# Kernel tuning notes

Measured on AMD Instinct MI355X. Metric: run time of the kernel, lower is better.

The kernel has to match this reference:

```python
import jax, jax.numpy as jnp
import numpy as np

B, SA, SB, H, D = 1, 2048, 512, 24, 128
DIM = H * D
EPS = 1e-6


def rms_norm(x, w):
    # fp32 variance as in the torch module (inputs already fp32 here)
    var = jnp.mean(jnp.square(x.astype(jnp.float32)), axis=-1, keepdims=True)
    y = (x * jax.lax.rsqrt(var + EPS)).astype(x.dtype)
    return y * w


def apply_rope(x, freqs):
    # x: [B,H,S,D]; freqs: [1,1,S,D/2,2,2]
    x_ = x.astype(jnp.float32).reshape(*x.shape[:-1], -1, 1, 2)  # [B,H,S,D/2,1,2]
    out = freqs[..., 0] * x_[..., 0] + freqs[..., 1] * x_[..., 1]  # [B,H,S,D/2,2]
    return out.reshape(x.shape).astype(x.dtype)


def qkv_split(x, W, b):
    # x: [B,S,DIM] -> q,k,v each [B,H,S,D]; chunk(3,dim=1) on 3H axis == major-3 split
    qkv = (x @ W + b).reshape(x.shape[0], x.shape[1], 3, H, D)
    qkv = jnp.transpose(qkv, (2, 0, 3, 1, 4))  # [3,B,H,S,D]
    return qkv[0], qkv[1], qkv[2]


def setup_inputs():
    key = jax.random.key(0)
    ks = jax.random.split(key, 8)
    s = 0.02
    return {
        "hidden_states_a": jax.random.normal(ks[0], (B, SA, DIM), jnp.float32),
        "hidden_states_b": jax.random.normal(ks[1], (B, SB, DIM), jnp.float32),
        "image_rotary_emb": jax.random.normal(ks[2], (1, 1, SA + SB, D // 2, 2, 2), jnp.float32),
        "Wqkv_a": jax.random.normal(ks[3], (DIM, 3 * DIM), jnp.float32) * s,
        "bqkv_a": jnp.zeros((3 * DIM,), jnp.float32),
        "Wqkv_b": jax.random.normal(ks[4], (DIM, 3 * DIM), jnp.float32) * s,
        "bqkv_b": jnp.zeros((3 * DIM,), jnp.float32),
        "wq_a": jnp.ones((D,), jnp.float32),
        "wk_a": jnp.ones((D,), jnp.float32),
        "wq_b": jnp.ones((D,), jnp.float32),
        "wk_b": jnp.ones((D,), jnp.float32),
        "Wout_a": jax.random.normal(ks[5], (DIM, DIM), jnp.float32) * s,
        "bout_a": jnp.zeros((DIM,), jnp.float32),
        "Wout_b": jax.random.normal(ks[6], (DIM, DIM), jnp.float32) * s,
        "bout_b": jnp.zeros((DIM,), jnp.float32),
    }


def reference(hidden_states_a, hidden_states_b, image_rotary_emb,
              Wqkv_a, bqkv_a, Wqkv_b, bqkv_b,
              wq_a, wk_a, wq_b, wk_b,
              Wout_a, bout_a, Wout_b, bout_b):
    q_a, k_a, v_a = qkv_split(hidden_states_a, Wqkv_a, bqkv_a)
    q_a, k_a = rms_norm(q_a, wq_a), rms_norm(k_a, wk_a)
    q_b, k_b, v_b = qkv_split(hidden_states_b, Wqkv_b, bqkv_b)
    q_b, k_b = rms_norm(q_b, wq_b), rms_norm(k_b, wk_b)

    q = jnp.concatenate([q_b, q_a], axis=2)
    k = jnp.concatenate([k_b, k_a], axis=2)
    v = jnp.concatenate([v_b, v_a], axis=2)
    q, k = apply_rope(q, image_rotary_emb), apply_rope(k, image_rotary_emb)

    scale = 1.0 / jnp.sqrt(jnp.asarray(D, q.dtype))
    scores = jnp.einsum("bhqd,bhkd->bhqk", q, k) * scale
    attn = jax.nn.softmax(scores, axis=-1)
    out = jnp.einsum("bhqk,bhkd->bhqd", attn, v)
    out = jnp.transpose(out, (0, 2, 1, 3)).reshape(B, SA + SB, DIM)

    out_b, out_a = out[:, :SB], out[:, SB:]
    hidden_states_a = out_a @ Wout_a + bout_a
    hidden_states_b = out_b @ Wout_b + bout_b
    return hidden_states_a, hidden_states_b
```

## Files before the change

kernel.cpp:

```cpp
#include <hip/hip_runtime.h>
#include <hip/hip_bf16.h>


typedef __attribute__((ext_vector_type(8))) short s16x8;
typedef __attribute__((ext_vector_type(8))) unsigned short u16x8;
typedef __attribute__((ext_vector_type(4))) unsigned short u16x4;
typedef __attribute__((ext_vector_type(4))) float f32x4;
typedef __attribute__((ext_vector_type(16))) float f32x16;

#define DEV static __device__ __forceinline__

#define S_TOT 2560
#define DIMC 3072
#define NQKV 9216

DEV unsigned short f2bf(float f) {
  union { float f; unsigned u; } v; v.f = f;
  return (unsigned short)((v.u + 0x7fffu + ((v.u >> 16) & 1u)) >> 16);
}
DEV float bf2f(unsigned short h) {
  union { unsigned u; float f; } v; v.u = ((unsigned)h) << 16;
  return v.f;
}
DEV void gload16(const void* g, void* l) {
  __builtin_amdgcn_global_load_lds((__attribute__((address_space(1))) void*)g,
                                   (__attribute__((address_space(3))) void*)l,
                                   16, 0, 0);
}
template <int N>
DEV void wait_vm() { asm volatile("s_waitcnt vmcnt(%0)" :: "n"(N) : "memory"); }
DEV float exp2_fast(float x) {
#if __has_builtin(__builtin_amdgcn_exp2f)
  return __builtin_amdgcn_exp2f(x);
#else
  return __expf(x * 0.69314718056f);
#endif
}

DEV void tile_map(int t, int mgrid, int* m, int* n) {
  int sg = t >> 4, loc = t & 15;
  int mgs = mgrid >> 2;
  int mg = sg % mgs, ng = sg / mgs;
  *m = mg * 4 + (loc & 3);
  *n = ng * 4 + (loc >> 2);
}


__global__ __launch_bounds__(256) void prep_all(
    const float* __restrict__ Wqa, const float* __restrict__ Wqb,
    const float* __restrict__ Woa, const float* __restrict__ Wob,
    const float* __restrict__ Xa, const float* __restrict__ Xb,
    unsigned short* __restrict__ Tqa, unsigned short* __restrict__ Tqb,
    unsigned short* __restrict__ Toa, unsigned short* __restrict__ Tob,
    unsigned short* __restrict__ Oa, unsigned short* __restrict__ Ob,
    int n8a, int n8b) {
  int id = blockIdx.x;
  if (id >= 18432) {
    int i = (id - 18432) * 256 + threadIdx.x;
    const float* in; unsigned short* out;
    if (i < n8a) { in = Xa; out = Oa; }
    else { i -= n8a; if (i >= n8b) return; in = Xb; out = Ob; }
    const float4* p = (const float4*)(in + (size_t)i * 8);
    float4 a = p[0], b = p[1];
    u16x8 u;
    u[0] = f2bf(a.x); u[1] = f2bf(a.y); u[2] = f2bf(a.z); u[3] = f2bf(a.w);
    u[4] = f2bf(b.x); u[5] = f2bf(b.y); u[6] = f2bf(b.z); u[7] = f2bf(b.w);
    *(u16x8*)(out + (size_t)i * 8) = u;
    return;
  }
  __shared__ float tile[64][65];
  const float* W; unsigned short* WT; int N, ncols;
  if (id < 6912)        { W = Wqa; WT = Tqa; N = NQKV; ncols = 144; }
  else if (id < 13824)  { W = Wqb; WT = Tqb; N = NQKV; ncols = 144; id -= 6912; }
  else if (id < 16128)  { W = Woa; WT = Toa; N = DIMC; ncols = 48;  id -= 13824; }
  else                  { W = Wob; WT = Tob; N = DIMC; ncols = 48;  id -= 16128; }
  const int t = threadIdx.x;
  const int n0 = (id % ncols) * 64, k0 = (id / ncols) * 64;
#pragma unroll
  for (int rep = 0; rep < 4; ++rep) {
    int idx = rep * 256 + t;
    int r = idx >> 4, c4 = (idx & 15) * 4;
    float4 v = *(const float4*)&W[(size_t)(k0 + r) * N + n0 + c4];
    tile[r][c4] = v.x; tile[r][c4 + 1] = v.y; tile[r][c4 + 2] = v.z; tile[r][c4 + 3] = v.w;
  }
  __syncthreads();
#pragma unroll
  for (int rep = 0; rep < 2; ++rep) {
    int idx = rep * 256 + t;
    int j = idx >> 3, i0 = (idx & 7) * 8;
    u16x8 u;
#pragma unroll
    for (int i = 0; i < 8; i++) u[i] = f2bf(tile[i0 + i][j]);
    *(u16x8*)&WT[(size_t)(n0 + j) * DIMC + k0 + i0] = u;
  }
}


struct StageSmem {
  unsigned short A[128 * 64];
  unsigned short B[128 * 64];
};

DEV void stage_tile(const char* A, const char* B, StageSmem* s, int kt, int tid) {
  const int row_s = tid >> 3;
  const int kbp = (tid & 7) * 16;
#pragma unroll
  for (int st = 0; st < 4; ++st) {
    int row = st * 32 + row_s;
    int kb = kbp ^ ((row & 7) << 4);
    gload16(A + (size_t)row * (DIMC * 2) + kt * 128 + kb, (char*)s->A + st * 4096 + tid * 16);
    gload16(B + (size_t)row * (DIMC * 2) + kt * 128 + kb, (char*)s->B + st * 4096 + tid * 16);
  }
}

DEV void compute_tile(const StageSmem* s, int wr, int wc, int lh, int ll,
                      f32x4 (&acc)[4][4]) {
#pragma unroll
  for (int ks = 0; ks < 2; ++ks) {
    s16x8 a[4], b[4];
#pragma unroll
    for (int f = 0; f < 4; ++f) {
      int ar = wr * 64 + f * 16 + ll;
      a[f] = *(const s16x8*)((const char*)s->A + ar * 128 +
                             ((ks * 64 + lh * 16) ^ ((ar & 7) << 4)));
      int br = wc * 64 + f * 16 + ll;
      b[f] = *(const s16x8*)((const char*)s->B + br * 128 +
                             ((ks * 64 + lh * 16) ^ ((br & 7) << 4)));
    }
#pragma unroll
    for (int i = 0; i < 4; i++)
#pragma unroll
      for (int j = 0; j < 4; j++)
        acc[i][j] = __builtin_amdgcn_mfma_f32_16x16x32_bf16(a[i], b[j], acc[i][j], 0, 0, 0);
  }
}

DEV void gemm_core_db(const unsigned short* __restrict__ Ap,
                      const unsigned short* __restrict__ Bp,
                      StageSmem (&sm)[2], int tid, f32x4 (&acc)[4][4]) {
  const int wave = tid >> 6, lane = tid & 63;
  const int wr = wave >> 1, wc = wave & 1;
  const int lh = lane >> 4, ll = lane & 15;

  stage_tile((const char*)Ap, (const char*)Bp, &sm[0], 0, tid);
  __syncthreads();
  for (int kt = 0; kt < 48; ++kt) {
    if (kt + 1 < 48)
      stage_tile((const char*)Ap, (const char*)Bp, &sm[(kt + 1) & 1], kt + 1, tid);
    compute_tile(&sm[kt & 1], wr, wc, lh, ll, acc);
    __syncthreads();
  }
}


union QkvSmem {
  StageSmem st[2];
  unsigned short ctile[128 * 136];
};

__global__ __launch_bounds__(256, 2) void qkv_gemm(
    const unsigned short* __restrict__ X0, const unsigned short* __restrict__ X1,
    const unsigned short* __restrict__ W0, const unsigned short* __restrict__ W1,
    const float* __restrict__ b0, const float* __restrict__ b1,
    const float* __restrict__ wqa, const float* __restrict__ wka,
    const float* __restrict__ wqb, const float* __restrict__ wkb,
    const float* __restrict__ freqs,
    unsigned short* __restrict__ Qb, unsigned short* __restrict__ Kb,
    unsigned short* __restrict__ Vt, int nt0) {
  __shared__ QkvSmem sm;
  const int tid = threadIdx.x;

  const int chunk = gridDim.x >> 3;
  const int nid = ((int)blockIdx.x & 7) * chunk + ((int)blockIdx.x >> 3);
  const int strm = (nid >= nt0) ? 1 : 0;
  const int t = strm ? nid - nt0 : nid;
  int mt, nt;
  tile_map(t, strm ? 4 : 16, &mt, &nt);
  const int m0 = mt * 128, n0 = nt * 128;
  const unsigned short* Xp = (strm ? X1 : X0) + (size_t)m0 * DIMC;
  const unsigned short* Wp = (strm ? W1 : W0) + (size_t)n0 * DIMC;
  const float* biasp = (strm ? b1 : b0);
  const int s_off = strm ? 0 : 512;

  f32x4 acc[4][4] = {};
  gemm_core_db(Xp, Wp, sm.st, tid, acc);

  {
    const int wave = tid >> 6, lane = tid & 63;
    const int wr = wave >> 1, wc = wave & 1, lh = lane >> 4, ll = lane & 15;
#pragma unroll
    for (int fn = 0; fn < 4; ++fn) {
      int c = wc * 64 + fn * 16 + ll;
      float bv = biasp[n0 + c];
#pragma unroll
      for (int fm = 0; fm < 4; ++fm)
#pragma unroll
        for (int j = 0; j < 4; j++) {
          int r = wr * 64 + fm * 16 + lh * 4 + j;
          sm.ctile[r * 136 + c] = f2bf(acc[fm][fn][j] + bv);
        }
    }
  }
  __syncthreads();

  const int qkv_idx = nt / 24;
  const int head = nt % 24;

  if (qkv_idx == 2) {
    const int sg0 = s_off + m0;
#pragma unroll
    for (int half = 0; half < 2; ++half) {
      int d = half * 64 + (tid >> 2);
      int t0 = (tid & 3) * 32;
      size_t obase = (size_t)(head * 128 + d) * S_TOT + sg0 + t0;
#pragma unroll
      for (int v = 0; v < 4; ++v) {
        u16x8 u;
#pragma unroll
        for (int i = 0; i < 8; i++) u[i] = sm.ctile[(t0 + v * 8 + i) * 136 + d];
        *(u16x8*)&Vt[obase + v * 8] = u;
      }
    }
  } else {
    const float* wn = (qkv_idx == 0) ? (strm ? wqb : wqa) : (strm ? wkb : wka);
    unsigned short* Ob = (qkv_idx == 0) ? Qb : Kb;
    const int row = tid >> 1, half = tid & 1;
    const int sg = s_off + m0 + row;
    float x[64];
    float ss = 0.f;
#pragma unroll
    for (int i = 0; i < 64; i++) {
      float v = bf2f(sm.ctile[row * 136 + half * 64 + i]);
      x[i] = v; ss += v * v;
    }
    ss += __shfl_xor(ss, 1);
    const float rn = rsqrtf(ss * (1.f / 128.f) + 1e-6f);
    const float* fr = freqs + (size_t)sg * 256 + half * 128;
    unsigned short o[64];
#pragma unroll
    for (int p = 0; p < 32; ++p) {
      float w0 = wn[half * 64 + 2 * p], w1 = wn[half * 64 + 2 * p + 1];
      float y0 = x[2 * p] * rn * w0, y1 = x[2 * p + 1] * rn * w1;
      float f00 = fr[p * 4], f01 = fr[p * 4 + 1], f10 = fr[p * 4 + 2], f11 = fr[p * 4 + 3];
      o[2 * p] = f2bf(f00 * y0 + f01 * y1);
      o[2 * p + 1] = f2bf(f10 * y0 + f11 * y1);
    }
    size_t ob = ((size_t)head * S_TOT + sg) * 128 + half * 64;
#pragma unroll
    for (int v = 0; v < 8; ++v) {
      u16x8 u;
#pragma unroll
      for (int i = 0; i < 8; i++) u[i] = o[v * 8 + i];
      *(u16x8*)&Ob[ob + v * 8] = u;
    }
  }
}


__global__ __launch_bounds__(256, 2) void out_gemm(
    const unsigned short* __restrict__ A0, const unsigned short* __restrict__ A1,
    const unsigned short* __restrict__ W0, const unsigned short* __restrict__ W1,
    const float* __restrict__ b0, const float* __restrict__ b1,
    float* __restrict__ C0, float* __restrict__ C1, int nt0) {
  __shared__ StageSmem sm[2];
  const int tid = threadIdx.x;
  const int chunk = gridDim.x >> 3;
  const int nid = ((int)blockIdx.x & 7) * chunk + ((int)blockIdx.x >> 3);
  const int strm = (nid >= nt0) ? 1 : 0;
  const int t = strm ? nid - nt0 : nid;
  int mt, nt;
  tile_map(t, strm ? 4 : 16, &mt, &nt);
  const int m0 = mt * 128, n0 = nt * 128;
  const unsigned short* Ap = (strm ? A1 : A0) + (size_t)m0 * DIMC;
  const unsigned short* Wp = (strm ? W1 : W0) + (size_t)n0 * DIMC;
  const float* bias = strm ? b1 : b0;
  float* C = strm ? C1 : C0;

  f32x4 acc[4][4] = {};
  gemm_core_db(Ap, Wp, sm, tid, acc);
  const int wave = tid >> 6, lane = tid & 63;
  const int wr = wave >> 1, wc = wave & 1, lh = lane >> 4, ll = lane & 15;
#pragma unroll
  for (int fn = 0; fn < 4; ++fn) {
    int c = n0 + wc * 64 + fn * 16 + ll;
    float bv = bias[c];
#pragma unroll
    for (int fm = 0; fm < 4; ++fm)
#pragma unroll
      for (int j = 0; j < 4; j++) {
        int r = m0 + wr * 64 + fm * 16 + lh * 4 + j;
        C[(size_t)r * DIMC + c] = acc[fm][fn][j] + bv;
      }
  }
}


__global__ __launch_bounds__(512, 1) void attn_k(
    const unsigned short* __restrict__ Qb, const unsigned short* __restrict__ Kb,
    const unsigned short* __restrict__ Vt, unsigned short* __restrict__ AO) {
  __shared__ alignas(128) unsigned short Ks[2][64 * 128];
  __shared__ alignas(128) unsigned short Vs[128 * 64];
  __shared__ alignas(128) unsigned short Ps[8][32 * 72];
  __shared__ float tabA[8][32];
  __shared__ float tabL[8][32];

  const int tid = threadIdx.x, w = tid >> 6, lane = tid & 63;
  const int lh = lane >> 4, ll16 = lane & 15;
  const int ll31 = lane & 31, hi = lane >> 5;
  const int wgid = blockIdx.x;
  const int nid = (wgid & 7) * 30 + (wgid >> 3);
  const int h = nid / 10, qt = nid % 10;
  const float C = 0.12751744f;

  s16x8 qf[2][4];
#pragma unroll
  for (int rb = 0; rb < 2; rb++) {
    size_t qbase = ((size_t)h * S_TOT + qt * 256 + w * 32 + rb * 16 + ll16) * 128;
#pragma unroll
    for (int ks = 0; ks < 4; ks++) qf[rb][ks] = *(const s16x8*)&Qb[qbase + ks * 32 + lh * 8];
  }

  float m2[2], l_r[2];
  f32x16 o[4] = {};
  m2[0] = m2[1] = -1e30f;
  l_r[0] = l_r[1] = 0.f;

  const unsigned short* Kh = Kb + (size_t)h * S_TOT * 128;
  const unsigned short* Vh = Vt + (size_t)h * 128 * S_TOT;
  unsigned short* Pw = &Ps[w][0];

  {
#pragma unroll
    for (int st = 0; st < 2; ++st) {
      int row = st * 32 + (tid >> 4);
      int col = ((tid & 15) * 16) ^ ((row & 7) << 4);
      gload16((const char*)(Kh + (size_t)row * 128) + col,
              (char*)&Ks[0][0] + (st * 512 + tid) * 16);
    }
  }

  int cur = 0;
  for (int kt = 0; kt < 40; ++kt) {
    wait_vm<0>();
    __builtin_amdgcn_s_barrier();
    {
      const int k0 = kt * 64;
#pragma unroll
      for (int st = 0; st < 2; ++st) {
        int row = st * 64 + (tid >> 3);
        int col = ((tid & 7) * 16) ^ ((row & 7) << 4);
        gload16((const char*)(Vh + (size_t)row * S_TOT + k0) + col,
                (char*)Vs + (st * 512 + tid) * 16);
      }
    }
    if (kt + 1 < 40) {
      const unsigned short* Kn = Kh + (size_t)(kt + 1) * 64 * 128;
#pragma unroll
      for (int st = 0; st < 2; ++st) {
        int row = st * 32 + (tid >> 4);
        int col = ((tid & 15) * 16) ^ ((row & 7) << 4);
        gload16((const char*)(Kn + (size_t)row * 128) + col,
                (char*)&Ks[cur ^ 1][0] + (st * 512 + tid) * 16);
      }
    }

    const char* Kc = (const char*)&Ks[cur][0];
    f32x4 sc[2][4] = {};
#pragma unroll
    for (int kb = 0; kb < 4; kb++) {
      int krow = kb * 16 + ll16;
      const char* kr = Kc + krow * 256;
      int swz = (krow & 7) << 4;
#pragma unroll
      for (int ks = 0; ks < 4; ks++) {
        s16x8 bf = *(const s16x8*)(kr + ((ks * 64 + lh * 16) ^ swz));
        sc[0][kb] = __builtin_amdgcn_mfma_f32_16x16x32_bf16(bf, qf[0][ks], sc[0][kb], 0, 0, 0);
        sc[1][kb] = __builtin_amdgcn_mfma_f32_16x16x32_bf16(bf, qf[1][ks], sc[1][kb], 0, 0, 0);
      }
    }

    float pmax[2];
#pragma unroll
    for (int rb = 0; rb < 2; rb++) {
      float v0 = fmaxf(fmaxf(sc[rb][0][0], sc[rb][0][1]), fmaxf(sc[rb][0][2], sc[rb][0][3]));
      float v1 = fmaxf(fmaxf(sc[rb][1][0], sc[rb][1][1]), fmaxf(sc[rb][1][2], sc[rb][1][3]));
      float v2 = fmaxf(fmaxf(sc[rb][2][0], sc[rb][2][1]), fmaxf(sc[rb][2][2], sc[rb][2][3]));
      float v3 = fmaxf(fmaxf(sc[rb][3][0], sc[rb][3][1]), fmaxf(sc[rb][3][2], sc[rb][3][3]));
      float v = fmaxf(fmaxf(v0, v1), fmaxf(v2, v3));
      v = fmaxf(v, __shfl_xor(v, 16));
      v = fmaxf(v, __shfl_xor(v, 32));
      pmax[rb] = v * C;
    }
    bool need = (pmax[0] > m2[0] + 8.0f) | (pmax[1] > m2[1] + 8.0f);
    if (__any(need)) {
#pragma unroll
      for (int rb = 0; rb < 2; rb++) {
        float mn = fmaxf(m2[rb], pmax[rb]);
        float al = exp2_fast(m2[rb] - mn);
        m2[rb] = mn;
        l_r[rb] *= al;
        if (lane < 16) tabA[w][rb * 16 + lane] = al;
      }
#pragma unroll
      for (int reg = 0; reg < 16; reg++) {
        int cr = (reg & 3) + 8 * (reg >> 2) + 4 * hi;
        float alv = tabA[w][cr];
        o[0][reg] *= alv; o[1][reg] *= alv; o[2][reg] *= alv; o[3][reg] *= alv;
      }
    }
#pragma unroll
    for (int rb = 0; rb < 2; rb++) {
      float ps = 0.f;
#pragma unroll
      for (int kb = 0; kb < 4; kb++) {
        float p0 = exp2_fast(sc[rb][kb][0] * C - m2[rb]);
        float p1 = exp2_fast(sc[rb][kb][1] * C - m2[rb]);
        float p2 = exp2_fast(sc[rb][kb][2] * C - m2[rb]);
        float p3 = exp2_fast(sc[rb][kb][3] * C - m2[rb]);
        ps += (p0 + p1) + (p2 + p3);
        u16x4 pk;
        pk[0] = f2bf(p0); pk[1] = f2bf(p1); pk[2] = f2bf(p2); pk[3] = f2bf(p3);
        *(u16x4*)((char*)Pw + (rb * 16 + ll16) * 144 + kb * 32 + lh * 8) = pk;
      }
      ps += __shfl_xor(ps, 16);
      ps += __shfl_xor(ps, 32);
      l_r[rb] += ps;
    }

    if (kt + 1 < 40) wait_vm<2>(); else wait_vm<0>();
    __builtin_amdgcn_s_barrier();

#pragma unroll
    for (int kstep = 0; kstep < 4; kstep++) {
      s16x8 pa = *(const s16x8*)((const char*)Pw + ll31 * 144 + kstep * 32 + hi * 16);
#pragma unroll
      for (int dblk = 0; dblk < 4; dblk++) {
        int vrow = dblk * 32 + ll31;
        s16x8 vb = *(const s16x8*)((const char*)Vs + vrow * 128 +
                                   ((kstep * 32 + hi * 16) ^ ((vrow & 7) << 4)));
        o[dblk] = __builtin_amdgcn_mfma_f32_32x32x16_bf16(pa, vb, o[dblk], 0, 0, 0);
      }
    }
    cur ^= 1;
  }

  if (lane < 16) {
    tabL[w][lane] = l_r[0];
    tabL[w][16 + lane] = l_r[1];
  }
#pragma unroll
  for (int reg = 0; reg < 16; reg++) {
    int cr = (reg & 3) + 8 * (reg >> 2) + 4 * hi;
    float inv = 1.0f / tabL[w][cr];
    int srow = qt * 256 + w * 32 + cr;
    size_t base = (size_t)srow * DIMC + h * 128;
#pragma unroll
    for (int dblk = 0; dblk < 4; dblk++)
      AO[base + dblk * 32 + ll31] = f2bf(o[dblk][reg] * inv);
  }
}


extern "C" void kernel_launch(void* const* d_in, const int* in_sizes, int n_in,
                              void* d_out, int out_size, void* d_ws, size_t ws_size,
                              hipStream_t stream) {
  (void)in_sizes; (void)n_in; (void)out_size; (void)ws_size;
  const float* Xa = (const float*)d_in[0];
  const float* Xb = (const float*)d_in[1];
  const float* freqs = (const float*)d_in[2];
  const float* Wqkv_a = (const float*)d_in[3];
  const float* bqkv_a = (const float*)d_in[4];
  const float* Wqkv_b = (const float*)d_in[5];
  const float* bqkv_b = (const float*)d_in[6];
  const float* wq_a = (const float*)d_in[7];
  const float* wk_a = (const float*)d_in[8];
  const float* wq_b = (const float*)d_in[9];
  const float* wk_b = (const float*)d_in[10];
  const float* Wout_a = (const float*)d_in[11];
  const float* bout_a = (const float*)d_in[12];
  const float* Wout_b = (const float*)d_in[13];
  const float* bout_b = (const float*)d_in[14];
  float* out = (float*)d_out;

  char* ws = (char*)d_ws;
  unsigned short* WTa  = (unsigned short*)ws; ws += (size_t)NQKV * DIMC * 2;
  unsigned short* WTb  = (unsigned short*)ws; ws += (size_t)NQKV * DIMC * 2;
  unsigned short* WoTa = (unsigned short*)ws; ws += (size_t)DIMC * DIMC * 2;
  unsigned short* WoTb = (unsigned short*)ws; ws += (size_t)DIMC * DIMC * 2;
  unsigned short* Xa16 = (unsigned short*)ws; ws += (size_t)2048 * DIMC * 2;
  unsigned short* Xb16 = (unsigned short*)ws; ws += (size_t)512 * DIMC * 2;
  unsigned short* Qb   = (unsigned short*)ws; ws += (size_t)24 * S_TOT * 128 * 2;
  unsigned short* Kbf  = (unsigned short*)ws; ws += (size_t)24 * S_TOT * 128 * 2;
  unsigned short* Vt   = (unsigned short*)ws; ws += (size_t)24 * S_TOT * 128 * 2;
  unsigned short* AO   = (unsigned short*)ws; ws += (size_t)S_TOT * DIMC * 2;

  const int n8a = 2048 * DIMC / 8, n8b = 512 * DIMC / 8;
  const int cvt_blocks = (n8a + n8b) / 256;
  prep_all<<<dim3(18432 + cvt_blocks), dim3(256), 0, stream>>>(
      Wqkv_a, Wqkv_b, Wout_a, Wout_b, Xa, Xb,
      WTa, WTb, WoTa, WoTb, Xa16, Xb16, n8a, n8b);

  qkv_gemm<<<dim3(1440), dim3(256), 0, stream>>>(Xa16, Xb16, WTa, WTb, bqkv_a, bqkv_b,
                                                 wq_a, wk_a, wq_b, wk_b, freqs,
                                                 Qb, Kbf, Vt, 1152);

  attn_k<<<dim3(240), dim3(512), 0, stream>>>(Qb, Kbf, Vt, AO);

  out_gemm<<<dim3(480), dim3(256), 0, stream>>>(AO + (size_t)512 * DIMC, AO, WoTa, WoTb,
                                                bout_a, bout_b, out,
                                                out + (size_t)2048 * DIMC, 384);
}
```

Baseline: 450.7 us.

## Split attention KV range in two, double Q rows per wave, add combine kernel

Each attention workgroup now covers 512 query rows (64 per wave) against half of the key/value sequence instead of 256 rows against the full sequence. Partial outputs, running maxima and sums go to a workspace, and a new combine kernel merges the two halves into AO. Doubling the query rows per wave reuses each K/V tile loaded into LDS twice as much. The exp/P write is interleaved with the QK MFMAs, and the lazy rescale now runs after the PV product. The cost is an extra kernel launch, extra global traffic for bf16 partials, higher register pressure, and an added bf16 rounding step on the partial outputs.

```diff
diff --git a/kernel.cpp b/kernel.cpp
--- a/kernel.cpp
+++ b/kernel.cpp
@@ -13,6 +13,7 @@
 #define S_TOT 2560
 #define DIMC 3072
 #define NQKV 9216
+#define NRQ (24 * 2560)
 
 DEV unsigned short f2bf(float f) {
   union { float f; unsigned u; } v; v.f = f;
@@ -297,36 +298,38 @@
 
 __global__ __launch_bounds__(512, 1) void attn_k(
     const unsigned short* __restrict__ Qb, const unsigned short* __restrict__ Kb,
-    const unsigned short* __restrict__ Vt, unsigned short* __restrict__ AO) {
+    const unsigned short* __restrict__ Vt, unsigned short* __restrict__ Opart,
+    float* __restrict__ Mpart, float* __restrict__ Lpart) {
   __shared__ alignas(128) unsigned short Ks[2][64 * 128];
   __shared__ alignas(128) unsigned short Vs[128 * 64];
-  __shared__ alignas(128) unsigned short Ps[8][32 * 72];
-  __shared__ float tabA[8][32];
-  __shared__ float tabL[8][32];
+  __shared__ alignas(128) unsigned short Ps[8][64 * 72];
+  __shared__ float tabA[8][64];
+  __shared__ float tabL[8][64];
 
   const int tid = threadIdx.x, w = tid >> 6, lane = tid & 63;
-  const int lh = lane >> 4, ll16 = lane & 15;
+  const int lh = (lane >> 4) & 3, ll16 = lane & 15;
   const int ll31 = lane & 31, hi = lane >> 5;
   const int wgid = blockIdx.x;
   const int nid = (wgid & 7) * 30 + (wgid >> 3);
-  const int h = nid / 10, qt = nid % 10;
+  const int h = nid / 10, rem = nid % 10;
+  const int qt = rem >> 1, kvh = rem & 1;
   const float C = 0.12751744f;
 
-  s16x8 qf[2][4];
-#pragma unroll
-  for (int rb = 0; rb < 2; rb++) {
-    size_t qbase = ((size_t)h * S_TOT + qt * 256 + w * 32 + rb * 16 + ll16) * 128;
+  s16x8 qf[4][4];
+#pragma unroll
+  for (int rb = 0; rb < 4; rb++) {
+    size_t qbase = ((size_t)h * S_TOT + qt * 512 + w * 64 + rb * 16 + ll16) * 128;
 #pragma unroll
     for (int ks = 0; ks < 4; ks++) qf[rb][ks] = *(const s16x8*)&Qb[qbase + ks * 32 + lh * 8];
   }
 
-  float m2[2], l_r[2];
-  f32x16 o[4] = {};
-  m2[0] = m2[1] = -1e30f;
-  l_r[0] = l_r[1] = 0.f;
-
-  const unsigned short* Kh = Kb + (size_t)h * S_TOT * 128;
-  const unsigned short* Vh = Vt + (size_t)h * 128 * S_TOT;
+  float m2[4], l_r[4];
+  f32x16 o[2][4] = {};
+#pragma unroll
+  for (int rb = 0; rb < 4; rb++) { m2[rb] = 0.f; l_r[rb] = 0.f; }
+
+  const unsigned short* Kh = Kb + ((size_t)h * S_TOT + kvh * 1280) * 128;
+  const unsigned short* Vh = Vt + (size_t)h * 128 * S_TOT + kvh * 1280;
   unsigned short* Pw = &Ps[w][0];
 
   {
@@ -340,7 +343,7 @@
   }
 
   int cur = 0;
-  for (int kt = 0; kt < 40; ++kt) {
+  for (int kt = 0; kt < 20; ++kt) {
     wait_vm<0>();
     __builtin_amdgcn_s_barrier();
     {
@@ -353,7 +356,7 @@
                 (char*)Vs + (st * 512 + tid) * 16);
       }
     }
-    if (kt + 1 < 40) {
+    if (kt + 1 < 20) {
       const unsigned short* Kn = Kh + (size_t)(kt + 1) * 64 * 128;
 #pragma unroll
       for (int st = 0; st < 2; ++st) {
@@ -365,36 +368,71 @@
     }
 
     const char* Kc = (const char*)&Ks[cur][0];
-    f32x4 sc[2][4] = {};
+    float vmax[4] = {-1e30f, -1e30f, -1e30f, -1e30f};
+    float psum[4] = {0.f, 0.f, 0.f, 0.f};
 #pragma unroll
     for (int kb = 0; kb < 4; kb++) {
+      f32x4 sc[4] = {};
       int krow = kb * 16 + ll16;
       const char* kr = Kc + krow * 256;
       int swz = (krow & 7) << 4;
 #pragma unroll
       for (int ks = 0; ks < 4; ks++) {
         s16x8 bf = *(const s16x8*)(kr + ((ks * 64 + lh * 16) ^ swz));
-        sc[0][kb] = __builtin_amdgcn_mfma_f32_16x16x32_bf16(bf, qf[0][ks], sc[0][kb], 0, 0, 0);
-        sc[1][kb] = __builtin_amdgcn_mfma_f32_16x16x32_bf16(bf, qf[1][ks], sc[1][kb], 0, 0, 0);
-      }
-    }
-
-    float pmax[2];
-#pragma unroll
-    for (int rb = 0; rb < 2; rb++) {
-      float v0 = fmaxf(fmaxf(sc[rb][0][0], sc[rb][0][1]), fmaxf(sc[rb][0][2], sc[rb][0][3]));
-      float v1 = fmaxf(fmaxf(sc[rb][1][0], sc[rb][1][1]), fmaxf(sc[rb][1][2], sc[rb][1][3]));
-      float v2 = fmaxf(fmaxf(sc[rb][2][0], sc[rb][2][1]), fmaxf(sc[rb][2][2], sc[rb][2][3]));
-      float v3 = fmaxf(fmaxf(sc[rb][3][0], sc[rb][3][1]), fmaxf(sc[rb][3][2], sc[rb][3][3]));
-      float v = fmaxf(fmaxf(v0, v1), fmaxf(v2, v3));
+#pragma unroll
+        for (int rb = 0; rb < 4; rb++)
+          sc[rb] = __builtin_amdgcn_mfma_f32_16x16x32_bf16(bf, qf[rb][ks], sc[rb], 0, 0, 0);
+      }
+#pragma unroll
+      for (int rb = 0; rb < 4; rb++) {
+        float mx = fmaxf(fmaxf(sc[rb][0], sc[rb][1]), fmaxf(sc[rb][2], sc[rb][3]));
+        vmax[rb] = fmaxf(vmax[rb], mx);
+        float p0 = exp2_fast(sc[rb][0] * C - m2[rb]);
+        float p1 = exp2_fast(sc[rb][1] * C - m2[rb]);
+        float p2 = exp2_fast(sc[rb][2] * C - m2[rb]);
+        float p3 = exp2_fast(sc[rb][3] * C - m2[rb]);
+        psum[rb] += (p0 + p1) + (p2 + p3);
+        u16x4 pk;
+        pk[0] = f2bf(p0); pk[1] = f2bf(p1); pk[2] = f2bf(p2); pk[3] = f2bf(p3);
+        *(u16x4*)((char*)Pw + (rb * 16 + ll16) * 144 + kb * 32 + lh * 8) = pk;
+      }
+    }
+    float pmax[4];
+#pragma unroll
+    for (int rb = 0; rb < 4; rb++) {
+      float ps = psum[rb];
+      ps += __shfl_xor(ps, 16);
+      ps += __shfl_xor(ps, 32);
+      l_r[rb] += ps;
+      float v = vmax[rb] * C;
       v = fmaxf(v, __shfl_xor(v, 16));
       v = fmaxf(v, __shfl_xor(v, 32));
-      pmax[rb] = v * C;
-    }
-    bool need = (pmax[0] > m2[0] + 8.0f) | (pmax[1] > m2[1] + 8.0f);
+      pmax[rb] = v;
+    }
+
+    if (kt + 1 < 20) wait_vm<2>(); else wait_vm<0>();
+    __builtin_amdgcn_s_barrier();
+
+#pragma unroll
+    for (int kstep = 0; kstep < 4; kstep++) {
+      s16x8 pa0 = *(const s16x8*)((const char*)Pw + ll31 * 144 + kstep * 32 + hi * 16);
+      s16x8 pa1 = *(const s16x8*)((const char*)Pw + (32 + ll31) * 144 + kstep * 32 + hi * 16);
+#pragma unroll
+      for (int dblk = 0; dblk < 4; dblk++) {
+        int vrow = dblk * 32 + ll31;
+        s16x8 vb = *(const s16x8*)((const char*)Vs + vrow * 128 +
+                                   ((kstep * 32 + hi * 16) ^ ((vrow & 7) << 4)));
+        o[0][dblk] = __builtin_amdgcn_mfma_f32_32x32x16_bf16(pa0, vb, o[0][dblk], 0, 0, 0);
+        o[1][dblk] = __builtin_amdgcn_mfma_f32_32x32x16_bf16(pa1, vb, o[1][dblk], 0, 0, 0);
+      }
+    }
+
+    bool need = false;
+#pragma unroll
+    for (int rb = 0; rb < 4; rb++) need |= (pmax[rb] > m2[rb] + 8.0f);
     if (__any(need)) {
 #pragma unroll
-      for (int rb = 0; rb < 2; rb++) {
+      for (int rb = 0; rb < 4; rb++) {
         float mn = fmaxf(m2[rb], pmax[rb]);
         float al = exp2_fast(m2[rb] - mn);
         m2[rb] = mn;
@@ -402,62 +440,63 @@
         if (lane < 16) tabA[w][rb * 16 + lane] = al;
       }
 #pragma unroll
-      for (int reg = 0; reg < 16; reg++) {
-        int cr = (reg & 3) + 8 * (reg >> 2) + 4 * hi;
-        float alv = tabA[w][cr];
-        o[0][reg] *= alv; o[1][reg] *= alv; o[2][reg] *= alv; o[3][reg] *= alv;
-      }
-    }
-#pragma unroll
-    for (int rb = 0; rb < 2; rb++) {
-      float ps = 0.f;
-#pragma unroll
-      for (int kb = 0; kb < 4; kb++) {
-        float p0 = exp2_fast(sc[rb][kb][0] * C - m2[rb]);
-        float p1 = exp2_fast(sc[rb][kb][1] * C - m2[rb]);
-        float p2 = exp2_fast(sc[rb][kb][2] * C - m2[rb]);
-        float p3 = exp2_fast(sc[rb][kb][3] * C - m2[rb]);
-        ps += (p0 + p1) + (p2 + p3);
-        u16x4 pk;
-        pk[0] = f2bf(p0); pk[1] = f2bf(p1); pk[2] = f2bf(p2); pk[3] = f2bf(p3);
-        *(u16x4*)((char*)Pw + (rb * 16 + ll16) * 144 + kb * 32 + lh * 8) = pk;
-      }
-      ps += __shfl_xor(ps, 16);
-      ps += __shfl_xor(ps, 32);
-      l_r[rb] += ps;
-    }
-
-    if (kt + 1 < 40) wait_vm<2>(); else wait_vm<0>();
-    __builtin_amdgcn_s_barrier();
-
-#pragma unroll
-    for (int kstep = 0; kstep < 4; kstep++) {
-      s16x8 pa = *(const s16x8*)((const char*)Pw + ll31 * 144 + kstep * 32 + hi * 16);
-#pragma unroll
-      for (int dblk = 0; dblk < 4; dblk++) {
-        int vrow = dblk * 32 + ll31;
-        s16x8 vb = *(const s16x8*)((const char*)Vs + vrow * 128 +
-                                   ((kstep * 32 + hi * 16) ^ ((vrow & 7) << 4)));
-        o[dblk] = __builtin_amdgcn_mfma_f32_32x32x16_bf16(pa, vb, o[dblk], 0, 0, 0);
-      }
+      for (int qb = 0; qb < 2; qb++)
+#pragma unroll
+        for (int reg = 0; reg < 16; reg++) {
+          int cr = (reg & 3) + 8 * (reg >> 2) + 4 * hi;
+          float alv = tabA[w][qb * 32 + cr];
+          o[qb][0][reg] *= alv; o[qb][1][reg] *= alv;
+          o[qb][2][reg] *= alv; o[qb][3][reg] *= alv;
+        }
     }
     cur ^= 1;
   }
 
   if (lane < 16) {
-    tabL[w][lane] = l_r[0];
-    tabL[w][16 + lane] = l_r[1];
-  }
-#pragma unroll
-  for (int reg = 0; reg < 16; reg++) {
-    int cr = (reg & 3) + 8 * (reg >> 2) + 4 * hi;
-    float inv = 1.0f / tabL[w][cr];
-    int srow = qt * 256 + w * 32 + cr;
-    size_t base = (size_t)srow * DIMC + h * 128;
-#pragma unroll
-    for (int dblk = 0; dblk < 4; dblk++)
-      AO[base + dblk * 32 + ll31] = f2bf(o[dblk][reg] * inv);
-  }
+#pragma unroll
+    for (int rb = 0; rb < 4; rb++) tabL[w][rb * 16 + lane] = l_r[rb];
+  }
+  const size_t prow0 = (size_t)(kvh * 24 + h) * 2560 + qt * 512 + w * 64;
+#pragma unroll
+  for (int qb = 0; qb < 2; qb++)
+#pragma unroll
+    for (int reg = 0; reg < 16; reg++) {
+      int cr = (reg & 3) + 8 * (reg >> 2) + 4 * hi;
+      float inv = 1.0f / tabL[w][qb * 32 + cr];
+      size_t base = (prow0 + qb * 32 + cr) * 128;
+#pragma unroll
+      for (int dblk = 0; dblk < 4; dblk++)
+        Opart[base + dblk * 32 + ll31] = f2bf(o[qb][dblk][reg] * inv);
+    }
+  if (lane < 16) {
+#pragma unroll
+    for (int rb = 0; rb < 4; rb++) {
+      size_t r = prow0 + rb * 16 + lane;
+      Mpart[r] = m2[rb];
+      Lpart[r] = l_r[rb];
+    }
+  }
+}
+
+
+__global__ __launch_bounds__(256) void combine_k(
+    const unsigned short* __restrict__ Opart, const float* __restrict__ Mpart,
+    const float* __restrict__ Lpart, unsigned short* __restrict__ AO) {
+  int idx = blockIdx.x * 256 + threadIdx.x;
+  int row = idx >> 4, d0 = (idx & 15) * 8;
+  float m1 = Mpart[row], mB = Mpart[NRQ + row];
+  float l1 = Lpart[row], lB = Lpart[NRQ + row];
+  float mm = fmaxf(m1, mB);
+  float w1 = exp2_fast(m1 - mm) * l1, w2 = exp2_fast(mB - mm) * lB;
+  float inv = 1.0f / (w1 + w2);
+  w1 *= inv; w2 *= inv;
+  u16x8 a = *(const u16x8*)&Opart[(size_t)row * 128 + d0];
+  u16x8 b = *(const u16x8*)&Opart[((size_t)NRQ + row) * 128 + d0];
+  int h = row / 2560, s = row % 2560;
+  u16x8 u;
+#pragma unroll
+  for (int i = 0; i < 8; i++) u[i] = f2bf(bf2f(a[i]) * w1 + bf2f(b[i]) * w2);
+  *(u16x8*)&AO[(size_t)s * DIMC + h * 128 + d0] = u;
 }
 
 
@@ -493,6 +532,9 @@
   unsigned short* Kbf  = (unsigned short*)ws; ws += (size_t)24 * S_TOT * 128 * 2;
   unsigned short* Vt   = (unsigned short*)ws; ws += (size_t)24 * S_TOT * 128 * 2;
   unsigned short* AO   = (unsigned short*)ws; ws += (size_t)S_TOT * DIMC * 2;
+  unsigned short* Opart = (unsigned short*)ws; ws += (size_t)2 * NRQ * 128 * 2;
+  float* Mpart = (float*)ws; ws += (size_t)2 * NRQ * 4;
+  float* Lpart = (float*)ws; ws += (size_t)2 * NRQ * 4;
 
   const int n8a = 2048 * DIMC / 8, n8b = 512 * DIMC / 8;
   const int cvt_blocks = (n8a + n8b) / 256;
@@ -504,7 +546,8 @@
                                                  wq_a, wk_a, wq_b, wk_b, freqs,
                                                  Qb, Kbf, Vt, 1152);
 
-  attn_k<<<dim3(240), dim3(512), 0, stream>>>(Qb, Kbf, Vt, AO);
+  attn_k<<<dim3(240), dim3(512), 0, stream>>>(Qb, Kbf, Vt, Opart, Mpart, Lpart);
+  combine_k<<<dim3(NRQ * 16 / 256), dim3(256), 0, stream>>>(Opart, Mpart, Lpart, AO);
 
   out_gemm<<<dim3(480), dim3(256), 0, stream>>>(AO + (size_t)512 * DIMC, AO, WoTa, WoTb,
                                                 bout_a, bout_b, out,
```

Result: slower. 652.5 us (+44.8%).
